# Kernel tuning notes

Hardware: AMD Instinct MI355X
Metric: run time of the kernel (lower is better)

The kernel has to match this reference:

```python
import jax, jax.numpy as jnp
import numpy as np
from jax import lax

WINDOW_SIZE = 11
SIGMA = 1.5
CHANNEL = 1
C1 = 0.01 ** 2
C2 = 0.03 ** 2


def _gaussian_1d(size, sigma):
    coords = jnp.arange(size, dtype=jnp.float32) - size // 2
    g = jnp.exp(-coords ** 2 / (2.0 * sigma ** 2))
    return g / g.sum()


def create_window_3d(window_size, channel, sigma=SIGMA):
    g = _gaussian_1d(window_size, sigma)
    # outer products -> (ws, ws, ws), normalized 3D Gaussian
    w3 = jnp.einsum('i,j,k->ijk', g, g, g)
    # (channel, 1, ws, ws, ws) for grouped (depthwise) conv, OIDHW layout
    return jnp.broadcast_to(w3[None, None], (channel, 1, window_size, window_size, window_size))


def _conv3d(x, window, channel):
    # padding window_size//2 with odd window == SAME
    return lax.conv_general_dilated(
        x, window,
        window_strides=(1, 1, 1),
        padding='SAME',
        feature_group_count=channel,
        dimension_numbers=('NCDHW', 'OIDHW', 'NCDHW'))


def setup_inputs() -> dict:
    key = jax.random.key(0)
    k1, k2 = jax.random.split(key)
    shape = (4, CHANNEL, 128, 128, 128)
    img1 = jax.random.uniform(k1, shape, dtype=jnp.float32)
    img2 = jax.random.uniform(k2, shape, dtype=jnp.float32)
    window = create_window_3d(WINDOW_SIZE, CHANNEL)
    return {"img1": img1, "img2": img2, "window": window}


def reference(img1, img2, window):
    channel = img1.shape[1]
    mu1 = _conv3d(img1, window, channel)
    mu2 = _conv3d(img2, window, channel)
    mu1_sq = mu1 * mu1
    mu2_sq = mu2 * mu2
    mu1_mu2 = mu1 * mu2
    sigma1_sq = _conv3d(img1 * img1, window, channel) - mu1_sq
    sigma2_sq = _conv3d(img2 * img2, window, channel) - mu2_sq
    sigma12 = _conv3d(img1 * img2, window, channel) - mu1_mu2
    ssim_map = ((2 * mu1_mu2 + C1) * (2 * sigma12 + C2)) / (
        (mu1_sq + mu2_sq + C1) * (sigma1_sq + sigma2_sq + C2))
    return ssim_map.mean()  # size_average=True
```

## Files before the change

### kernel.cpp

```cpp
#include <hip/hip_runtime.h>


#define SLICE (128*128)
#define S  (128*SLICE)
#define C1_ 0.0001f
#define C2_ 0.0009f

__device__ __forceinline__ void make_g_s(float* gs) {
    float g[11]; float s = 0.f;
#pragma unroll
    for (int i = 0; i < 11; ++i) {
        float d = (float)(i - 5);
        g[i] = __expf(-d * d / 4.5f);
        s += g[i];
    }
    float inv = 1.f / s;
#pragma unroll
    for (int i = 0; i < 11; ++i)
        gs[i] = __int_as_float(__builtin_amdgcn_readfirstlane(
                    __float_as_int(g[i] * inv)));
}

#define RB    160
#define RSLOT (2*RB)
#define WRING (4*RSLOT)

#define STEPA(T_, TM_, J0_, J1_, STORE_, OKC_, RPE_, WPE_) do {               \
    const int T__ = (T_);                                                     \
    int sp__ = T__ + 3; if (sp__ > 41) sp__ = 41;                             \
    int rowc__ = min(max(y0 + sp__ - 5, 0), 127);                             \
    float4 Rn__ = *(const float4*)(src + (size_t)rowc__ * 128);               \
    if (OKC_) {                                                               \
        const float* rp__ = (RPE_);                                           \
        float v1__[12], v2__[12];                                             \
        _Pragma("unroll")                                                     \
        for (int j = 0; j < 12; ++j) {                                        \
            v1__[j] = rp__[j]; v2__[j] = rp__[RB + j];                        \
        }                                                                     \
        float u1__ = 0.f, u2__ = 0.f, a11__ = 0.f, a22__ = 0.f, a12__ = 0.f;  \
        _Pragma("unroll")                                                     \
        for (int j = 0; j < 11; ++j) {                                        \
            float wj__ = gs[j];                                               \
            float av__ = v1__[j], bv__ = v2__[j];                             \
            float ta__ = wj__ * av__, tb__ = wj__ * bv__;                     \
            u1__ += ta__; u2__ += tb__;                                       \
            a11__ = fmaf(ta__, av__, a11__);                                  \
            a12__ = fmaf(ta__, bv__, a12__);                                  \
            a22__ = fmaf(tb__, bv__, a22__);                                  \
        }                                                                     \
        _Pragma("unroll")                                                     \
        for (int j = (J0_); j <= (J1_); ++j) {                                \
            const int sl__ = ((TM_) + j + 1) % 11;                            \
            float wy__ = gs[10 - j];                                          \
            acc[0][sl__] = fmaf(wy__, u1__,  acc[0][sl__]);                   \
            acc[1][sl__] = fmaf(wy__, u2__,  acc[1][sl__]);                   \
            acc[2][sl__] = fmaf(wy__, a11__, acc[2][sl__]);                   \
            acc[3][sl__] = fmaf(wy__, a22__, acc[3][sl__]);                   \
            acc[4][sl__] = fmaf(wy__, a12__, acc[4][sl__]);                   \
        }                                                                     \
    }                                                                         \
    *(float4*)(WPE_) = h1;            \
    if (STORE_) {                                                             \
        const int es__ = ((TM_) + 1) % 11;                                    \
        size_t wo__ = (size_t)(y0 + T__ - 10) * 128;                          \
        _Pragma("unroll")                                                     \
        for (int f = 0; f < 5; ++f) {                                         \
            fb[(size_t)f * S + wo__] = acc[f][es__];                          \
            acc[f][es__] = 0.f;                                               \
        }                                                                     \
    }                                                                         \
    h1 = h2; h2 = Rn__;                                                       \
} while (0)

__global__ __launch_bounds__(128, 2)
void ssimA(const float* __restrict__ img1, const float* __restrict__ img2,
           float* __restrict__ fields) {
    __shared__ __align__(16) float ring[2 * WRING];
    float gs[11]; make_g_s(gs);
    const int x = threadIdx.x;
    const int w = x >> 6, l = x & 63;
    const int b = blockIdx.x;
    const int yc = b & 3, z = (b >> 2) & 127, n = b >> 9;
    const int y0 = yc * 32;
    const float* src = (l < 32 ? img1 : img2)
                     + (size_t)n * S + (size_t)z * SLICE + 4 * (l & 31);
    float* fb = fields + (size_t)n * 5 * S + (size_t)z * SLICE + x;

    float* wring = ring + w * WRING;
    float* p_rd = wring + (x + 3);
    float* p_wr = wring + ((l < 32) ? 0 : RB) + 8 + 4 * (l & 31);

    for (int i = l; i < WRING; i += 64) wring[i] = 0.f;

    float acc[5][11];
#pragma unroll
    for (int f = 0; f < 5; ++f)
#pragma unroll
        for (int s2 = 0; s2 < 11; ++s2) acc[f][s2] = 0.f;

    float4 h1, h2;
    {
        int r0 = min(max(y0 - 5, 0), 127);
        int r1 = min(max(y0 - 4, 0), 127);
        int r2 = min(max(y0 - 3, 0), 127);
        float4 R0 = *(const float4*)(src + (size_t)r0 * 128);
        h1        = *(const float4*)(src + (size_t)r1 * 128);
        h2        = *(const float4*)(src + (size_t)r2 * 128);
        *(float4*)(p_wr) = R0;
    }

#pragma unroll
    for (int t = 0; t < 10; ++t) {
        STEPA(t, t, 10 - t, 10, false, (y0 + t - 5 >= 0),
              p_rd + (t & 3) * RSLOT, p_wr + ((t + 1) & 3) * RSLOT);
    }
    {
        int ro = 2 * RSLOT, wro = 3 * RSLOT;
#pragma unroll 1
        for (int blk = 0; blk < 2; ++blk) {
#pragma unroll
            for (int tt = 0; tt < 11; ++tt) {
                STEPA(10 + blk * 11 + tt, 10 + tt, 0, 10, true, true,
                      p_rd + ro, p_wr + wro);
                ro = wro;
                wro += RSLOT; if (wro == WRING) wro = 0;
            }
        }
    }
#pragma unroll
    for (int t = 32; t < 42; ++t) {
        STEPA(t, t % 11, 0, 41 - t, true, (y0 + t - 5 < 128),
              p_rd + (t & 3) * RSLOT, p_wr + ((t + 1) & 3) * RSLOT);
    }
}

#define STEPB(T_, TM_, J0_, J1_, STORE_, OKC_) do {                           \
    const int T__ = (T_);                                                     \
    int sp__ = T__ + 4; if (sp__ > 41) sp__ = 41;                             \
    size_t off__ = (size_t)min(max(z0 + sp__ - 5, 0), 127) * SLICE;           \
    float N__[5];                                                             \
    _Pragma("unroll")                                                         \
    for (int f = 0; f < 5; ++f) N__[f] = base[(size_t)f * S + off__];         \
    if (OKC_) {                                                               \
        _Pragma("unroll")                                                     \
        for (int j = (J0_); j <= (J1_); ++j) {                                \
            const int sl__ = ((TM_) + j + 1) % 11;                            \
            float wz__ = gs[10 - j];                                          \
            acc[0][sl__] = fmaf(wz__, P0[0], acc[0][sl__]);                   \
            acc[1][sl__] = fmaf(wz__, P0[1], acc[1][sl__]);                   \
            acc[2][sl__] = fmaf(wz__, P0[2], acc[2][sl__]);                   \
            acc[3][sl__] = fmaf(wz__, P0[3], acc[3][sl__]);                   \
            acc[4][sl__] = fmaf(wz__, P0[4], acc[4][sl__]);                   \
        }                                                                     \
    }                                                                         \
    if (STORE_) {                                                             \
        const int es__ = ((TM_) + 1) % 11;                                    \
        float m1__ = acc[0][es__], m2__ = acc[1][es__];                       \
        float p11__ = acc[2][es__], p22__ = acc[3][es__], p12__ = acc[4][es__];\
        float m1s__ = m1__ * m1__, m2s__ = m2__ * m2__, m12__ = m1__ * m2__;  \
        float v1c__ = p11__ - m1s__, v2c__ = p22__ - m2s__, cv__ = p12__ - m12__;\
        float num__ = (2.f * m12__ + C1_) * (2.f * cv__ + C2_);               \
        float den__ = (m1s__ + m2s__ + C1_) * (v1c__ + v2c__ + C2_);          \
        sum += num__ / den__;                                                 \
        _Pragma("unroll")                                                     \
        for (int f = 0; f < 5; ++f) acc[f][es__] = 0.f;                       \
    }                                                                         \
    _Pragma("unroll")                                                         \
    for (int f = 0; f < 5; ++f) {                                             \
        P0[f] = P1[f]; P1[f] = P2[f]; P2[f] = P3[f]; P3[f] = N__[f];          \
    }                                                                         \
} while (0)

__global__ __launch_bounds__(256, 1)
void ssimB(const float* __restrict__ fields, float* __restrict__ partials) {
    float gs[11]; make_g_s(gs);
    const int tid = threadIdx.x;
    const int x = tid & 127, yr = tid >> 7;
    const int b = blockIdx.x;
    const int zc = b & 3, y2 = (b >> 2) & 63;
    const int n = 3 - (b >> 8);
    const int y = y2 * 2 + yr;
    const int z0 = zc * 32;
    const float* base = fields + (size_t)n * 5 * S + (size_t)y * 128 + x;

    float acc[5][11];
#pragma unroll
    for (int f = 0; f < 5; ++f)
#pragma unroll
        for (int s2 = 0; s2 < 11; ++s2) acc[f][s2] = 0.f;

    float sum = 0.f;

    float P0[5], P1[5], P2[5], P3[5];
    {
        size_t o0 = (size_t)min(max(z0 - 5, 0), 127) * SLICE;
        size_t o1 = (size_t)min(max(z0 - 4, 0), 127) * SLICE;
        size_t o2 = (size_t)min(max(z0 - 3, 0), 127) * SLICE;
        size_t o3 = (size_t)min(max(z0 - 2, 0), 127) * SLICE;
#pragma unroll
        for (int f = 0; f < 5; ++f) {
            P0[f] = base[(size_t)f * S + o0];
            P1[f] = base[(size_t)f * S + o1];
            P2[f] = base[(size_t)f * S + o2];
            P3[f] = base[(size_t)f * S + o3];
        }
    }

#pragma unroll
    for (int t = 0; t < 10; ++t) {
        STEPB(t, t, 10 - t, 10, false, (z0 + t - 5 >= 0));
    }
#pragma unroll 1
    for (int blk = 0; blk < 2; ++blk) {
#pragma unroll
        for (int tt = 0; tt < 11; ++tt) {
            STEPB(10 + blk * 11 + tt, 10 + tt, 0, 10, true, true);
        }
    }
#pragma unroll
    for (int t = 32; t < 42; ++t) {
        STEPB(t, t % 11, 0, 41 - t, true, (z0 + t - 5 < 128));
    }

#pragma unroll
    for (int o = 32; o > 0; o >>= 1) sum += __shfl_down(sum, o, 64);
    __shared__ float ws4[4];
    if ((tid & 63) == 0) ws4[tid >> 6] = sum;
    __syncthreads();
    if (tid == 0) partials[blockIdx.x] = ws4[0] + ws4[1] + ws4[2] + ws4[3];
}

__global__ void ssim_final(const float* __restrict__ partial, int n,
                           float* __restrict__ out, double inv_count) {
    int tid = threadIdx.x;
    double s = 0.0;
    for (int i = tid; i < n; i += 256) s += (double)partial[i];
#pragma unroll
    for (int o = 32; o > 0; o >>= 1) s += __shfl_down(s, o, 64);
    __shared__ double wsum[4];
    int lane = tid & 63, wid = tid >> 6;
    if (lane == 0) wsum[wid] = s;
    __syncthreads();
    if (tid == 0)
        out[0] = (float)((wsum[0] + wsum[1] + wsum[2] + wsum[3]) * inv_count);
}

extern "C" void kernel_launch(void* const* d_in, const int* in_sizes, int n_in,
                              void* d_out, int out_size, void* d_ws, size_t ws_size,
                              hipStream_t stream) {
    const float* img1 = (const float*)d_in[0];
    const float* img2 = (const float*)d_in[1];
    float* out = (float*)d_out;

    float* fields   = (float*)d_ws;
    float* partials = fields + 20 * (size_t)S;

    ssimA<<<2048, 128, 0, stream>>>(img1, img2, fields);
    ssimB<<<1024, 256, 0, stream>>>(fields, partials);
    ssim_final<<<1, 256, 0, stream>>>(partials, 1024, out,
                                      1.0 / ((double)S * 4));
}
```

Before: 183.0 us.

## Interleave field planes per row, shrink LDS ring, vectorize x-window reads

Changes the intermediate field layout so the five fields sit next to each other inside each row (z, y, field, x) instead of in five separate volumes. Each thread's five stores and loads then fall in one contiguous 2.5KB row region, which improves locality and simplifies addressing. The x-direction window now reads float2 pairs from LDS at an even-aligned offset, using a per-thread shifted 12-tap weight array to cover odd alignment. The LDS ring shrinks from four slots to two, which cuts shared memory but assumes the double-buffered ordering is still safe without extra syncs.

```diff
diff --git a/kernel.cpp b/kernel.cpp
--- a/kernel.cpp
+++ b/kernel.cpp
@@ -3,6 +3,8 @@
 
 #define SLICE (128*128)
 #define S  (128*SLICE)
+#define ZROW 640
+#define ZSL  81920
 #define C1_ 0.0001f
 #define C2_ 0.0009f
 
@@ -23,7 +25,7 @@
 
 #define RB    160
 #define RSLOT (2*RB)
-#define WRING (4*RSLOT)
+#define WRING (2*RSLOT)
 
 #define STEPA(T_, TM_, J0_, J1_, STORE_, OKC_, RPE_, WPE_) do {               \
     const int T__ = (T_);                                                     \
@@ -32,21 +34,27 @@
     float4 Rn__ = *(const float4*)(src + (size_t)rowc__ * 128);               \
     if (OKC_) {                                                               \
         const float* rp__ = (RPE_);                                           \
-        float v1__[12], v2__[12];                                             \
-        _Pragma("unroll")                                                     \
-        for (int j = 0; j < 12; ++j) {                                        \
-            v1__[j] = rp__[j]; v2__[j] = rp__[RB + j];                        \
-        }                                                                     \
         float u1__ = 0.f, u2__ = 0.f, a11__ = 0.f, a22__ = 0.f, a12__ = 0.f;  \
         _Pragma("unroll")                                                     \
-        for (int j = 0; j < 11; ++j) {                                        \
-            float wj__ = gs[j];                                               \
-            float av__ = v1__[j], bv__ = v2__[j];                             \
-            float ta__ = wj__ * av__, tb__ = wj__ * bv__;                     \
-            u1__ += ta__; u2__ += tb__;                                       \
-            a11__ = fmaf(ta__, av__, a11__);                                  \
-            a12__ = fmaf(ta__, bv__, a12__);                                  \
-            a22__ = fmaf(tb__, bv__, a22__);                                  \
+        for (int j = 0; j < 6; ++j) {                                         \
+            float2 va__ = *(const float2*)(rp__ + 2 * j);                     \
+            float2 vb__ = *(const float2*)(rp__ + RB + 2 * j);                \
+            {                                                                 \
+                float wj__ = w12[2 * j];                                      \
+                float ta__ = wj__ * va__.x, tb__ = wj__ * vb__.x;             \
+                u1__ += ta__; u2__ += tb__;                                   \
+                a11__ = fmaf(ta__, va__.x, a11__);                            \
+                a12__ = fmaf(ta__, vb__.x, a12__);                            \
+                a22__ = fmaf(tb__, vb__.x, a22__);                            \
+            }                                                                 \
+            {                                                                 \
+                float wj__ = w12[2 * j + 1];                                  \
+                float ta__ = wj__ * va__.y, tb__ = wj__ * vb__.y;             \
+                u1__ += ta__; u2__ += tb__;                                   \
+                a11__ = fmaf(ta__, va__.y, a11__);                            \
+                a12__ = fmaf(ta__, vb__.y, a12__);                            \
+                a22__ = fmaf(tb__, vb__.y, a22__);                            \
+            }                                                                 \
         }                                                                     \
         _Pragma("unroll")                                                     \
         for (int j = (J0_); j <= (J1_); ++j) {                                \
@@ -61,11 +69,11 @@
     }                                                                         \
     *(float4*)(WPE_) = h1;            \
     if (STORE_) {                                                             \
+        size_t wo__ = (size_t)(y0 + T__ - 10) * ZROW;                         \
         const int es__ = ((TM_) + 1) % 11;                                    \
-        size_t wo__ = (size_t)(y0 + T__ - 10) * 128;                          \
         _Pragma("unroll")                                                     \
         for (int f = 0; f < 5; ++f) {                                         \
-            fb[(size_t)f * S + wo__] = acc[f][es__];                          \
+            fb[wo__ + f * 128] = acc[f][es__];                                \
             acc[f][es__] = 0.f;                                               \
         }                                                                     \
     }                                                                         \
@@ -84,10 +92,20 @@
     const int y0 = yc * 32;
     const float* src = (l < 32 ? img1 : img2)
                      + (size_t)n * S + (size_t)z * SLICE + 4 * (l & 31);
-    float* fb = fields + (size_t)n * 5 * S + (size_t)z * SLICE + x;
+    float* fb = fields + (size_t)(n * 128 + z) * ZSL + x;
+
+    const int p = (x - 5) & 1;
+    const int e = (x - 5) - p;
+    float w12[12];
+#pragma unroll
+    for (int k = 0; k < 12; ++k) {
+        float we = (k <= 10) ? gs[k] : 0.f;
+        float wo = (k >= 1) ? gs[k - 1] : 0.f;
+        w12[k] = p ? wo : we;
+    }
 
     float* wring = ring + w * WRING;
-    float* p_rd = wring + (x + 3);
+    float* p_rd = wring + (8 + e);
     float* p_wr = wring + ((l < 32) ? 0 : RB) + 8 + 4 * (l & 31);
 
     for (int i = l; i < WRING; i += 64) wring[i] = 0.f;
@@ -112,35 +130,36 @@
 #pragma unroll
     for (int t = 0; t < 10; ++t) {
         STEPA(t, t, 10 - t, 10, false, (y0 + t - 5 >= 0),
-              p_rd + (t & 3) * RSLOT, p_wr + ((t + 1) & 3) * RSLOT);
+              p_rd + (t & 1) * RSLOT, p_wr + ((t + 1) & 1) * RSLOT);
     }
     {
-        int ro = 2 * RSLOT, wro = 3 * RSLOT;
+        int ro = 0, wro = RSLOT;
 #pragma unroll 1
         for (int blk = 0; blk < 2; ++blk) {
 #pragma unroll
             for (int tt = 0; tt < 11; ++tt) {
                 STEPA(10 + blk * 11 + tt, 10 + tt, 0, 10, true, true,
                       p_rd + ro, p_wr + wro);
-                ro = wro;
-                wro += RSLOT; if (wro == WRING) wro = 0;
+                ro ^= RSLOT; wro ^= RSLOT;
             }
         }
     }
 #pragma unroll
     for (int t = 32; t < 42; ++t) {
         STEPA(t, t % 11, 0, 41 - t, true, (y0 + t - 5 < 128),
-              p_rd + (t & 3) * RSLOT, p_wr + ((t + 1) & 3) * RSLOT);
+              p_rd + (t & 1) * RSLOT, p_wr + ((t + 1) & 1) * RSLOT);
     }
 }
 
 #define STEPB(T_, TM_, J0_, J1_, STORE_, OKC_) do {                           \
     const int T__ = (T_);                                                     \
     int sp__ = T__ + 4; if (sp__ > 41) sp__ = 41;                             \
-    size_t off__ = (size_t)min(max(z0 + sp__ - 5, 0), 127) * SLICE;           \
-    float N__[5];                                                             \
-    _Pragma("unroll")                                                         \
-    for (int f = 0; f < 5; ++f) N__[f] = base[(size_t)f * S + off__];         \
+    size_t off__ = (size_t)min(max(z0 + sp__ - 5, 0), 127) * ZSL;             \
+    float N0__ = base[off__];                                                 \
+    float N1__ = base[off__ + 128];                                           \
+    float N2__ = base[off__ + 256];                                           \
+    float N3__ = base[off__ + 384];                                           \
+    float N4__ = base[off__ + 512];                                           \
     if (OKC_) {                                                               \
         _Pragma("unroll")                                                     \
         for (int j = (J0_); j <= (J1_); ++j) {                                \
@@ -166,9 +185,8 @@
         for (int f = 0; f < 5; ++f) acc[f][es__] = 0.f;                       \
     }                                                                         \
     _Pragma("unroll")                                                         \
-    for (int f = 0; f < 5; ++f) {                                             \
-        P0[f] = P1[f]; P1[f] = P2[f]; P2[f] = P3[f]; P3[f] = N__[f];          \
-    }                                                                         \
+    for (int f = 0; f < 5; ++f) { P0[f] = P1[f]; P1[f] = P2[f]; P2[f] = P3[f]; } \
+    P3[0] = N0__; P3[1] = N1__; P3[2] = N2__; P3[3] = N3__; P3[4] = N4__;     \
 } while (0)
 
 __global__ __launch_bounds__(256, 1)
@@ -181,7 +199,7 @@
     const int n = 3 - (b >> 8);
     const int y = y2 * 2 + yr;
     const int z0 = zc * 32;
-    const float* base = fields + (size_t)n * 5 * S + (size_t)y * 128 + x;
+    const float* base = fields + (size_t)n * 128 * ZSL + (size_t)y * ZROW + x;
 
     float acc[5][11];
 #pragma unroll
@@ -193,16 +211,16 @@
 
     float P0[5], P1[5], P2[5], P3[5];
     {
-        size_t o0 = (size_t)min(max(z0 - 5, 0), 127) * SLICE;
-        size_t o1 = (size_t)min(max(z0 - 4, 0), 127) * SLICE;
-        size_t o2 = (size_t)min(max(z0 - 3, 0), 127) * SLICE;
-        size_t o3 = (size_t)min(max(z0 - 2, 0), 127) * SLICE;
+        size_t o0 = (size_t)min(max(z0 - 5, 0), 127) * ZSL;
+        size_t o1 = (size_t)min(max(z0 - 4, 0), 127) * ZSL;
+        size_t o2 = (size_t)min(max(z0 - 3, 0), 127) * ZSL;
+        size_t o3 = (size_t)min(max(z0 - 2, 0), 127) * ZSL;
 #pragma unroll
         for (int f = 0; f < 5; ++f) {
-            P0[f] = base[(size_t)f * S + o0];
-            P1[f] = base[(size_t)f * S + o1];
-            P2[f] = base[(size_t)f * S + o2];
-            P3[f] = base[(size_t)f * S + o3];
+            P0[f] = base[o0 + f * 128];
+            P1[f] = base[o1 + f * 128];
+            P2[f] = base[o2 + f * 128];
+            P3[f] = base[o3 + f * 128];
         }
     }
 
```

Result: faster. 169.0 us (-7.6%).
